# Performance work log

Hardware: AMD Instinct MI355X
Metric: run time of the kernel (lower is better)

The kernel has to match this reference:

```python
import jax, jax.numpy as jnp
import numpy as np

HEADS, DIM_HEAD, BLOCK, EPS = 16, 64, 16, 1e-8


def _hattn(x, w_qkv, w_out, b_out):
    b, n, dim = x.shape
    h, dh, bsz = HEADS, DIM_HEAD, BLOCK
    scale = dh ** -0.5
    # n is a power of two, so the module's pad-to-pow2 step is a no-op.
    qkv = x @ w_qkv  # [b, n, 3*h*dh]
    q, k, v = jnp.split(qkv, 3, axis=-1)

    def to_heads(t):  # [b, n, h*dh] -> [(b h), n, dh]
        return t.reshape(b, n, h, dh).transpose(0, 2, 1, 3).reshape(b * h, n, dh)

    q, k, v = to_heads(q) * scale, to_heads(k), to_heads(v)

    num_levels = int(np.log2(n // bsz)) - 1
    levels = [(q, k, v)]
    for _ in range(num_levels):  # coarsen: mean-pool q,k; sum-pool v (mask=None path)
        q = q.reshape(b * h, -1, 2, dh).mean(axis=2)
        k = k.reshape(b * h, -1, 2, dh).mean(axis=2)
        v = v.reshape(b * h, -1, 2, dh).sum(axis=2)
        levels.append((q, k, v))

    def flip_blocks(t):  # swap adjacent blocks along the block axis: [B, nb, z, d]
        B, nb, z, d = t.shape
        return t.reshape(B, nb // 2, 2, z, d)[:, :, ::-1].reshape(B, nb, z, d)

    Ys = []
    last = len(levels) - 1
    for ind, (ql, kl, vl) in enumerate(reversed(levels)):  # coarsest -> finest
        B, N, d = ql.shape
        qb = ql.reshape(B, N // bsz, bsz, d)
        kb = vb = None
        kb = kl.reshape(B, N // bsz, bsz, d)
        vb = vl.reshape(B, N // bsz, bsz, d)
        if ind != last:  # off-diagonal pairing at coarse levels
            kb, vb = flip_blocks(kb), flip_blocks(vb)
        S = jnp.einsum('bnid,bnjd->bnij', qb, kb)
        S = S - S.max(axis=-1, keepdims=True)
        A = jnp.exp(S)
        y = jnp.einsum('bnij,bnjd->bnid', A, vb)
        Ys.append((y.reshape(B, N, d), A.sum(-1).reshape(B, N)))

    Y, Asum = Ys[0]
    for y_l, a_l in Ys[1:]:  # upsample-and-accumulate across levels
        Y = jnp.repeat(Y, 2, axis=1) + y_l
        Asum = jnp.repeat(Asum, 2, axis=1) + a_l

    out = Y / (Asum + EPS)[..., None]  # [(b h), n, dh]
    out = out.reshape(b, h, n, dh).transpose(0, 2, 1, 3).reshape(b, n, h * dh)
    return out @ w_out + b_out


def setup_inputs() -> dict:
    key = jax.random.key(0)
    k1, k2, k3 = jax.random.split(key, 3)
    b, n, dim = 4, 8192, 1024
    inner = HEADS * DIM_HEAD
    x = jax.random.normal(k1, (b, n, dim), dtype=jnp.float32)
    w_qkv = jax.random.normal(k2, (dim, inner * 3), dtype=jnp.float32) * 0.02
    w_out = jax.random.normal(k3, (inner, dim), dtype=jnp.float32) * 0.02
    b_out = jnp.zeros((dim,), dtype=jnp.float32)
    return {"x": x, "w_qkv": w_qkv, "w_out": w_out, "b_out": b_out}


def reference(x, w_qkv, w_out, b_out):
    return _hattn(x, w_qkv, w_out, b_out)
```

## Files before the change

### kernel.cpp

```cpp
#include <hip/hip_runtime.h>

typedef unsigned short u16;
typedef unsigned int u32;
typedef __bf16 bf16x8 __attribute__((ext_vector_type(8)));
typedef float f32x4 __attribute__((ext_vector_type(4)));

__device__ inline float bf2f(u16 u) { u32 x = ((u32)u) << 16; return __uint_as_float(x); }
__device__ inline u16 f2bf(float f) {
  u32 x = __float_as_uint(f);
  u32 r = (x + 0x7FFFu + ((x >> 16) & 1u)) >> 16;
  return (u16)r;
}
__device__ inline u32 pack2(float lo, float hi) {
  return (u32)f2bf(lo) | ((u32)f2bf(hi) << 16);
}

__global__ __launch_bounds__(256) void cast_bf16(const float* __restrict__ s,
                                                 u16* __restrict__ d, int n4) {
  const float4* s4 = (const float4*)s;
  u32* d2 = (u32*)d;
  int i = blockIdx.x * 256 + threadIdx.x;
  int stride = gridDim.x * 256;
  for (; i < n4; i += stride) {
    float4 f = s4[i];
    d2[2 * i]     = pack2(f.x, f.y);
    d2[2 * i + 1] = pack2(f.z, f.w);
  }
}

__global__ __launch_bounds__(256) void transpose_cast(const float* __restrict__ src,
                                                      u16* __restrict__ dst, int R, int C) {
  __shared__ float tile[32][33];
  int bx = blockIdx.x, by = blockIdx.y;
  int tx = threadIdx.x & 31, ty = threadIdx.x >> 5;
  for (int rr = ty; rr < 32; rr += 8)
    tile[rr][tx] = src[(size_t)(by * 32 + rr) * C + bx * 32 + tx];
  __syncthreads();
  for (int rr = ty; rr < 32; rr += 8)
    dst[(size_t)(bx * 32 + rr) * R + by * 32 + tx] = f2bf(tile[tx][rr]);
}

#define MFMAQ(AF, BF, MO, NO)                                                     \
  _Pragma("unroll") for (int mf = 0; mf < 4; ++mf)                                \
  _Pragma("unroll") for (int nf = 0; nf < 2; ++nf)                                \
  _Pragma("unroll") for (int kq = 0; kq < 2; ++kq)                                \
    acc[(MO) + mf][(NO) + nf] = __builtin_amdgcn_mfma_f32_16x16x32_bf16(          \
        AF[mf][kq], BF[nf][kq], acc[(MO) + mf][(NO) + nf], 0, 0, 0);

#define PH_OPEN12                                                                 \
  asm volatile("s_waitcnt lgkmcnt(8)" ::: "memory");                              \
  __builtin_amdgcn_s_barrier();                                                   \
  asm volatile("s_waitcnt lgkmcnt(0)" ::: "memory");                              \
  __builtin_amdgcn_sched_barrier(0);                                              \
  __builtin_amdgcn_s_setprio(1);

#define PH_OPEN                                                                   \
  __builtin_amdgcn_s_barrier();                                                   \
  asm volatile("s_waitcnt lgkmcnt(0)" ::: "memory");                              \
  __builtin_amdgcn_sched_barrier(0);                                              \
  __builtin_amdgcn_s_setprio(1);

#define PH_CLOSE                                                                  \
  __builtin_amdgcn_s_setprio(0);                                                  \
  __builtin_amdgcn_s_barrier();                                                   \
  __builtin_amdgcn_sched_barrier(0);

#define PH_CLOSE_VM                                                               \
  __builtin_amdgcn_s_setprio(0);                                                  \
  asm volatile("s_waitcnt vmcnt(4)" ::: "memory");                                \
  __builtin_amdgcn_s_barrier();                                                   \
  __builtin_amdgcn_sched_barrier(0);

template <int EPI>
__global__ __launch_bounds__(512, 2) void gemm8p(
    const u16* __restrict__ A, const u16* __restrict__ Bt, int M, int N, int K, int NB,
    u16* __restrict__ q0, u16* __restrict__ k0, u16* __restrict__ v0,
    u16* __restrict__ q4, u16* __restrict__ k4, u16* __restrict__ v4,
    float* __restrict__ out, const float* __restrict__ bias) {
  __shared__ u16 lds[2][2][16384];
  const int tid = threadIdx.x;
  const int lane = tid & 63;
  const int wave = tid >> 6;
  const int wm = wave >> 2, wn = wave & 3;
  const int lr = lane & 15, lg = lane >> 4;

  const int nwg = gridDim.x;
  const int bid = blockIdx.x;
  const int swz = (bid & 7) * (nwg >> 3) + (bid >> 3);
  const int m0 = (swz / NB) * 256;
  const int n0 = (swz % NB) * 256;
  const int NT = K >> 6;
  const int NI = NT >> 1;

  auto stage_half = [&](int buf, int ht, int kt_) {
    const u16* src = (ht < 2) ? A : Bt;
    const int r0 = (ht < 2) ? m0 : n0;
    u16* ldsop = &lds[buf][ht >> 1][0];
#pragma unroll
    for (int ii = 0; ii < 2; ++ii) {
      int c2 = ((ht & 1) * 2 + ii) * 512 + tid;
      int row = c2 >> 3, ps = c2 & 7;
      int ks = ps ^ (row & 7);
      const u16* g = src + (size_t)(r0 + row) * K + kt_ + ks * 8;
      char* l = (char*)ldsop + (size_t)((((ht & 1) * 2 + ii) * 512 + (tid & ~63)) * 16);
      __builtin_amdgcn_global_load_lds((const __attribute__((address_space(1))) void*)g,
                                       (__attribute__((address_space(3))) void*)l, 16, 0, 0);
    }
  };
  auto rdA = [&](int c, int mf, int kq) -> bf16x8 {
    int rl = wm * 128 + mf * 16 + lr;
    int sl = (kq * 4 + lg) ^ (rl & 7);
    return *(const bf16x8*)(&lds[c][0][rl * 64 + sl * 8]);
  };
  auto rdB = [&](int c, int nf, int kq) -> bf16x8 {
    int rl = wn * 64 + nf * 16 + lr;
    int sl = (kq * 4 + lg) ^ (rl & 7);
    return *(const bf16x8*)(&lds[c][1][rl * 64 + sl * 8]);
  };

  f32x4 acc[8][4];
#pragma unroll
  for (int mf = 0; mf < 8; ++mf)
#pragma unroll
    for (int nf = 0; nf < 4; ++nf) acc[mf][nf] = f32x4{0.f, 0.f, 0.f, 0.f};

  stage_half(0, 2, 0); stage_half(0, 3, 0); stage_half(0, 0, 0); stage_half(0, 1, 0);
  stage_half(1, 2, 64); stage_half(1, 3, 64);
  asm volatile("s_waitcnt vmcnt(4)" ::: "memory");
  __builtin_amdgcn_s_barrier();
  __builtin_amdgcn_sched_barrier(0);

  bf16x8 afA[4][2], afB[4][2], bA[2][2], bB[2][2];
  for (int it = 0; it < NI; ++it) {
    const int kO  = (2 * it + 1) << 6;
    const int t2  = 2 * it + 2, t3 = 2 * it + 3;
    const int kE2 = ((t2 < NT) ? t2 : NT - 1) << 6;
    const int kO2 = ((t3 < NT) ? t3 : NT - 1) << 6;

#pragma unroll
    for (int mf = 0; mf < 4; ++mf) { afA[mf][0] = rdA(0, mf, 0); afA[mf][1] = rdA(0, mf, 1); }
#pragma unroll
    for (int nf = 0; nf < 2; ++nf) { bA[nf][0] = rdB(0, nf, 0); bA[nf][1] = rdB(0, nf, 1); }
    stage_half(1, 0, kO);
    PH_OPEN12 MFMAQ(afA, bA, 0, 0) PH_CLOSE
#pragma unroll
    for (int nf = 0; nf < 2; ++nf) { bB[nf][0] = rdB(0, 2 + nf, 0); bB[nf][1] = rdB(0, 2 + nf, 1); }
    stage_half(1, 1, kO);
    PH_OPEN MFMAQ(afA, bB, 0, 2) PH_CLOSE
#pragma unroll
    for (int mf = 0; mf < 4; ++mf) { afB[mf][0] = rdA(0, 4 + mf, 0); afB[mf][1] = rdA(0, 4 + mf, 1); }
    stage_half(0, 2, kE2);
    PH_OPEN MFMAQ(afB, bB, 4, 2) PH_CLOSE
    stage_half(0, 3, kE2);
    PH_OPEN MFMAQ(afB, bA, 4, 0) PH_CLOSE_VM
#pragma unroll
    for (int mf = 0; mf < 4; ++mf) { afA[mf][0] = rdA(1, mf, 0); afA[mf][1] = rdA(1, mf, 1); }
#pragma unroll
    for (int nf = 0; nf < 2; ++nf) { bA[nf][0] = rdB(1, nf, 0); bA[nf][1] = rdB(1, nf, 1); }
    stage_half(0, 0, kE2);
    PH_OPEN12 MFMAQ(afA, bA, 0, 0) PH_CLOSE
#pragma unroll
    for (int nf = 0; nf < 2; ++nf) { bB[nf][0] = rdB(1, 2 + nf, 0); bB[nf][1] = rdB(1, 2 + nf, 1); }
    stage_half(0, 1, kE2);
    PH_OPEN MFMAQ(afA, bB, 0, 2) PH_CLOSE
#pragma unroll
    for (int mf = 0; mf < 4; ++mf) { afB[mf][0] = rdA(1, 4 + mf, 0); afB[mf][1] = rdA(1, 4 + mf, 1); }
    stage_half(1, 2, kO2);
    PH_OPEN MFMAQ(afB, bB, 4, 2) PH_CLOSE
    stage_half(1, 3, kO2);
    PH_OPEN MFMAQ(afB, bA, 4, 0) PH_CLOSE_VM
  }
  asm volatile("s_waitcnt vmcnt(0)" ::: "memory");

#pragma unroll
  for (int mf = 0; mf < 8; ++mf) {
#pragma unroll
    for (int nf = 0; nf < 4; ++nf) {
      int col = n0 + wn * 64 + nf * 16 + lr;
      if (EPI == 0) {
        int p = col >> 10, cc = col & 1023;
        int h = cc >> 6, d = cc & 63;
        u16* dst = (p == 0) ? q0 : (p == 1) ? k0 : v0;
        float sc = (p == 0) ? 0.125f : 1.0f;
#pragma unroll
        for (int jj = 0; jj < 4; ++jj) {
          int row = m0 + wm * 128 + mf * 16 + lg * 4 + jj;
          int b = row >> 13, nn = row & 8191;
          dst[((size_t)((b << 4) + h) * 8192 + nn) * 64 + d] = f2bf(acc[mf][nf][jj] * sc);
        }
        float s4 = acc[mf][nf][0] + acc[mf][nf][1] + acc[mf][nf][2] + acc[mf][nf][3];
        s4 += __shfl_xor(s4, 16);
        s4 += __shfl_xor(s4, 32);
        if (lane < 16) {
          int row = m0 + wm * 128 + mf * 16;
          int b = row >> 13, n4 = (row & 8191) >> 4;
          u16* dst4 = (p == 0) ? q4 : (p == 1) ? k4 : v4;
          float val = (p == 2) ? s4 : s4 * 0.0625f;
          if (p == 0) val *= 0.125f;
          dst4[((size_t)((b << 4) + h) * 512 + n4) * 64 + d] = f2bf(val);
        }
      } else {
        float bv = bias[col];
#pragma unroll
        for (int jj = 0; jj < 4; ++jj) {
          int row = m0 + wm * 128 + mf * 16 + lg * 4 + jj;
          out[(size_t)row * N + col] = acc[mf][nf][jj] + bv;
        }
      }
    }
  }
}

__global__ __launch_bounds__(256) void pool_all4(
    const u16* __restrict__ q4, const u16* __restrict__ k4, const u16* __restrict__ v4,
    u16* __restrict__ qd, u16* __restrict__ kd, u16* __restrict__ vd) {
  int t = blockIdx.x * 256 + threadIdx.x;
  if (t >= 983040) return;
  int arr = blockIdx.y;
  int col = t & 31;
  int rr = t >> 5;
  int Bi = rr / 480;
  int r = rr % 480;
  int base, w, Nl;
  if (r < 256)      { base = 0;   w = 2;  Nl = 256; }
  else if (r < 384) { base = 256; w = 4;  Nl = 128; r -= 256; }
  else if (r < 448) { base = 384; w = 8;  Nl = 64;  r -= 384; }
  else              { base = 448; w = 16; Nl = 32;  r -= 448; }
  const u32* s = (const u32*)(arr == 0 ? q4 : arr == 1 ? k4 : v4);
  const u32* src = s + ((size_t)Bi * 512 + (size_t)r * w) * 32 + col;
  float lo = 0, hi = 0;
  for (int m = 0; m < w; ++m) {
    u32 u = src[(size_t)m * 32];
    lo += bf2f((u16)u); hi += bf2f((u16)(u >> 16));
  }
  float sc = (arr == 2) ? 1.0f : (1.0f / (float)w);
  u32* d = (u32*)(arr == 0 ? qd : arr == 1 ? kd : vd);
  d[(size_t)2048 * base + ((size_t)Bi * Nl + r) * 32 + col] = pack2(lo * sc, hi * sc);
}

__global__ __launch_bounds__(256) void hattn_coarse(
    const u16* __restrict__ q4, const u16* __restrict__ k4, const u16* __restrict__ v4,
    const u16* __restrict__ qc, const u16* __restrict__ kc, const u16* __restrict__ vc,
    float* __restrict__ ylvl, float* __restrict__ alvl) {
  __shared__ float qs[16][68], ks[16][68], vs[16][68];
  __shared__ float As[16][17];
  const int bx = blockIdx.x, Bi = blockIdx.y;
  int lvl, jb;
  if (bx < 32)      { lvl = 0; jb = bx; }
  else if (bx < 48) { lvl = 1; jb = bx - 32; }
  else if (bx < 56) { lvl = 2; jb = bx - 48; }
  else if (bx < 60) { lvl = 3; jb = bx - 56; }
  else              { lvl = 4; jb = bx - 60; }
  const int N = 512 >> lvl;
  const int srcb[5] = {0, 0, 256, 384, 448};
  const int offr[5] = {0, 512, 768, 896, 960};
  const u16* qp = (lvl == 0) ? q4 : qc + (size_t)4096 * srcb[lvl];
  const u16* kp = (lvl == 0) ? k4 : kc + (size_t)4096 * srcb[lvl];
  const u16* vp = (lvl == 0) ? v4 : vc + (size_t)4096 * srcb[lvl];
  const int tid = threadIdx.x;
  const int jk = jb ^ 1;
  const u32* qg = (const u32*)(qp + ((size_t)Bi * N + jb * 16) * 64);
  const u32* kg = (const u32*)(kp + ((size_t)Bi * N + jk * 16) * 64);
  const u32* vg = (const u32*)(vp + ((size_t)Bi * N + jk * 16) * 64);
#pragma unroll
  for (int u = tid; u < 512; u += 256) {
    int row = u >> 5, dp = (u & 31) * 2;
    u32 a = qg[u]; qs[row][dp] = bf2f((u16)a); qs[row][dp + 1] = bf2f((u16)(a >> 16));
    u32 b = kg[u]; ks[row][dp] = bf2f((u16)b); ks[row][dp + 1] = bf2f((u16)(b >> 16));
    u32 c = vg[u]; vs[row][dp] = bf2f((u16)c); vs[row][dp + 1] = bf2f((u16)(c >> 16));
  }
  __syncthreads();
  const int i = tid >> 4, j = tid & 15;
  float s = 0.f;
  const float4* qv = (const float4*)&qs[i][0];
  const float4* kv = (const float4*)&ks[j][0];
#pragma unroll
  for (int d4 = 0; d4 < 16; ++d4) {
    float4 a = qv[d4], b = kv[d4];
    s += a.x * b.x + a.y * b.y + a.z * b.z + a.w * b.w;
  }
  float mx = s;
#pragma unroll
  for (int off = 8; off; off >>= 1) mx = fmaxf(mx, __shfl_xor(mx, off, 16));
  float aexp = __expf(s - mx);
  float asum = aexp;
#pragma unroll
  for (int off = 8; off; off >>= 1) asum += __shfl_xor(asum, off, 16);
  As[i][j] = aexp;
  __syncthreads();
  float y0 = 0, y1 = 0, y2 = 0, y3 = 0;
  const int d0 = j * 4;
#pragma unroll
  for (int jj = 0; jj < 16; ++jj) {
    float av = As[i][jj];
    const float4 vv = *(const float4*)&vs[jj][d0];
    y0 += av * vv.x; y1 += av * vv.y; y2 += av * vv.z; y3 += av * vv.w;
  }
  const int nf = jb * 16 + i;
  float* yo = ylvl + (size_t)4096 * offr[lvl] + ((size_t)Bi * N + nf) * 64 + d0;
  yo[0] = y0; yo[1] = y1; yo[2] = y2; yo[3] = y3;
  if (j == 0) alvl[(size_t)64 * offr[lvl] + (size_t)Bi * N + nf] = asum;
}

union F8 { u32 w[4]; bf16x8 v; };

__device__ inline void acc_row8(const u16* p, float* a) {
  const u32* qw = (const u32*)p;
#pragma unroll
  for (int m = 0; m < 4; ++m) {
    u32 u = qw[m];
    a[2 * m]     += bf2f((u16)u);
    a[2 * m + 1] += bf2f((u16)(u >> 16));
  }
}
__device__ inline bf16x8 mk8(const float* a, float s) {
  F8 f;
#pragma unroll
  for (int m = 0; m < 4; ++m) f.w[m] = pack2(a[2 * m] * s, a[2 * m + 1] * s);
  return f.v;
}
__device__ inline bf16x8 pool_frag(const u16* arr, int row0, int cnt, int slotq, float scale) {
  float a[8] = {0, 0, 0, 0, 0, 0, 0, 0};
  for (int m = 0; m < cnt; ++m) {
    int r = row0 + m;
    acc_row8(arr + r * 64 + ((slotq ^ (r & 7)) * 8), a);
  }
  return mk8(a, scale);
}
__device__ inline bf16x8 rd_frag(const u16* arr, int r, int slotq) {
  return *(const bf16x8*)(arr + r * 64 + ((slotq ^ (r & 7)) * 8));
}
template <int LVL>
__device__ inline bf16x8 vt_frag(const u16* Vt, int c, int rbase) {
  float a[8] = {0, 0, 0, 0, 0, 0, 0, 0};
  const u32* p = (const u32*)(Vt + c * 266 + rbase);
#pragma unroll
  for (int g = 0; g < (1 << LVL); ++g) {
#pragma unroll
    for (int m = 0; m < 4; ++m) {
      u32 u = p[g * 4 + m];
      int t = g * 8 + 2 * m;
      a[t >> LVL]       += bf2f((u16)u);
      a[(t + 1) >> LVL] += bf2f((u16)(u >> 16));
    }
  }
  return mk8(a, 1.0f);
}

__device__ inline bf16x8 qk_softmax(bf16x8 ka0, bf16x8 ka1, bf16x8 qb0, bf16x8 qb1,
                                    int lane, float* asum_out) {
  f32x4 s = {0.f, 0.f, 0.f, 0.f};
  s = __builtin_amdgcn_mfma_f32_16x16x32_bf16(ka0, qb0, s, 0, 0, 0);
  s = __builtin_amdgcn_mfma_f32_16x16x32_bf16(ka1, qb1, s, 0, 0, 0);
  float mx = fmaxf(fmaxf(s[0], s[1]), fmaxf(s[2], s[3]));
  mx = fmaxf(mx, __shfl_xor(mx, 32));
  mx = fmaxf(mx, __shfl_xor(mx, 16));
  float p0 = __expf(s[0] - mx), p1 = __expf(s[1] - mx);
  float p2 = __expf(s[2] - mx), p3 = __expf(s[3] - mx);
  float as = p0 + p1 + p2 + p3;
  as += __shfl_xor(as, 32);
  as += __shfl_xor(as, 16);
  *asum_out = as;
  u32 pk01 = pack2(p0, p1), pk23 = pack2(p2, p3);
  int jq = lane & 15, lg = lane >> 4;
  int a1 = ((((lg * 2) * 16) + jq) & 63) << 2;
  int a2 = ((((lg * 2 + 1) * 16) + jq) & 63) << 2;
  F8 f;
  f.w[0] = (u32)__builtin_amdgcn_ds_bpermute(a1, (int)pk01);
  f.w[1] = (u32)__builtin_amdgcn_ds_bpermute(a1, (int)pk23);
  f.w[2] = (u32)__builtin_amdgcn_ds_bpermute(a2, (int)pk01);
  f.w[3] = (u32)__builtin_amdgcn_ds_bpermute(a2, (int)pk23);
  if (lg >= 2) { f.w[0] = 0; f.w[1] = 0; f.w[2] = 0; f.w[3] = 0; }
  return f.v;
}

__global__ __launch_bounds__(512, 1) void attn_fine(
    const u16* __restrict__ q, const u16* __restrict__ k, const u16* __restrict__ v,
    const float* __restrict__ ylvl, const float* __restrict__ alvl,
    u16* __restrict__ outA) {
  __shared__ u16 Qs[16384];
  __shared__ u16 Ks[16384];
  __shared__ u16 Vt[17024];
  __shared__ float Yc1[128][68];
  __shared__ float Yc2[64][68];
  __shared__ float Yc3[32][68];
  __shared__ float SUMc[224];
  const int tid = threadIdx.x;
  const int lane = tid & 63;
  const int wv = tid >> 6;
  const int j = lane & 15, lg = lane >> 4;
  const int ci = blockIdx.x, Bi = blockIdx.y;
  const size_t gbase = ((size_t)Bi * 8192 + (size_t)ci * 256) * 64;

#pragma unroll
  for (int it = 0; it < 4; ++it) {
    int sidx = it * 512 + tid;
    int row = sidx >> 3, ps = sidx & 7;
    int ks_ = ps ^ (row & 7);
    const u16* gq = q + gbase + (size_t)row * 64 + ks_ * 8;
    const u16* gk = k + gbase + (size_t)row * 64 + ks_ * 8;
    char* lq = (char*)Qs + (size_t)(it * 512 + (tid & ~63)) * 16;
    char* lk = (char*)Ks + (size_t)(it * 512 + (tid & ~63)) * 16;
    __builtin_amdgcn_global_load_lds((const __attribute__((address_space(1))) void*)gq,
                                     (__attribute__((address_space(3))) void*)lq, 16, 0, 0);
    __builtin_amdgcn_global_load_lds((const __attribute__((address_space(1))) void*)gk,
                                     (__attribute__((address_space(3))) void*)lk, 16, 0, 0);
  }
  {
    const uint4* gv = (const uint4*)(v + gbase);
    u32* Vt32 = (u32*)Vt;
#pragma unroll
    for (int it = 0; it < 2; ++it) {
      int i = it * 512 + tid;
      int r2 = i >> 3, cg = i & 7, c0 = cg * 8;
      uint4 a = gv[(size_t)(2 * r2) * 8 + cg];
      uint4 b = gv[(size_t)(2 * r2 + 1) * 8 + cg];
      const u16* pa = (const u16*)&a;
      const u16* pb = (const u16*)&b;
#pragma unroll
      for (int m = 0; m < 8; ++m)
        Vt32[(c0 + m) * 133 + r2] = (u32)pa[m] | ((u32)pb[m] << 16);
    }
  }
  __syncthreads();

  {
    int kb = wv ^ 1;
    bf16x8 ka0 = pool_frag(Ks, kb * 32 + 2 * j, 2, lg, 0.5f);
    bf16x8 ka1 = pool_frag(Ks, kb * 32 + 2 * j, 2, 4 + lg, 0.5f);
    bf16x8 qb0 = pool_frag(Qs, wv * 32 + 2 * j, 2, lg, 0.5f);
    bf16x8 qb1 = pool_frag(Qs, wv * 32 + 2 * j, 2, 4 + lg, 0.5f);
    float as;
    bf16x8 pa = qk_softmax(ka0, ka1, qb0, qb1, lane, &as);
    if (lg == 0) SUMc[wv * 16 + j] = as;
    int rb = kb * 32 + (lg & 1) * 16;
    f32x4 acc[4];
#pragma unroll
    for (int ch = 0; ch < 4; ++ch) {
      bf16x8 vb = vt_frag<1>(Vt, ch * 16 + j, rb);
      acc[ch] = __builtin_amdgcn_mfma_f32_16x16x32_bf16(pa, vb, f32x4{0.f,0.f,0.f,0.f}, 0, 0, 0);
    }
#pragma unroll
    for (int ch = 0; ch < 4; ++ch)
#pragma unroll
      for (int jj = 0; jj < 4; ++jj)
        Yc1[wv * 16 + lg * 4 + jj][ch * 16 + j] = acc[ch][jj];
  }
  if (wv < 4) {
    int kb = wv ^ 1;
    bf16x8 ka0 = pool_frag(Ks, kb * 64 + 4 * j, 4, lg, 0.25f);
    bf16x8 ka1 = pool_frag(Ks, kb * 64 + 4 * j, 4, 4 + lg, 0.25f);
    bf16x8 qb0 = pool_frag(Qs, wv * 64 + 4 * j, 4, lg, 0.25f);
    bf16x8 qb1 = pool_frag(Qs, wv * 64 + 4 * j, 4, 4 + lg, 0.25f);
    float as;
    bf16x8 pa = qk_softmax(ka0, ka1, qb0, qb1, lane, &as);
    if (lg == 0) SUMc[128 + wv * 16 + j] = as;
    int rb = kb * 64 + (lg & 1) * 32;
    f32x4 acc[4];
#pragma unroll
    for (int ch = 0; ch < 4; ++ch) {
      bf16x8 vb = vt_frag<2>(Vt, ch * 16 + j, rb);
      acc[ch] = __builtin_amdgcn_mfma_f32_16x16x32_bf16(pa, vb, f32x4{0.f,0.f,0.f,0.f}, 0, 0, 0);
    }
#pragma unroll
    for (int ch = 0; ch < 4; ++ch)
#pragma unroll
      for (int jj = 0; jj < 4; ++jj)
        Yc2[wv * 16 + lg * 4 + jj][ch * 16 + j] = acc[ch][jj];
  }
  if (wv >= 6) {
    int w3 = wv - 6;
    int kb = w3 ^ 1;
    bf16x8 ka0 = pool_frag(Ks, kb * 128 + 8 * j, 8, lg, 0.125f);
    bf16x8 ka1 = pool_frag(Ks, kb * 128 + 8 * j, 8, 4 + lg, 0.125f);
    bf16x8 qb0 = pool_frag(Qs, w3 * 128 + 8 * j, 8, lg, 0.125f);
    bf16x8 qb1 = pool_frag(Qs, w3 * 128 + 8 * j, 8, 4 + lg, 0.125f);
    float as;
    bf16x8 pa = qk_softmax(ka0, ka1, qb0, qb1, lane, &as);
    if (lg == 0) SUMc[192 + w3 * 16 + j] = as;
    int rb = kb * 128 + (lg & 1) * 64;
    f32x4 acc[4];
#pragma unroll
    for (int ch = 0; ch < 4; ++ch) {
      bf16x8 vb = vt_frag<3>(Vt, ch * 16 + j, rb);
      acc[ch] = __builtin_amdgcn_mfma_f32_16x16x32_bf16(pa, vb, f32x4{0.f,0.f,0.f,0.f}, 0, 0, 0);
    }
#pragma unroll
    for (int ch = 0; ch < 4; ++ch)
#pragma unroll
      for (int jj = 0; jj < 4; ++jj)
        Yc3[w3 * 16 + lg * 4 + jj][ch * 16 + j] = acc[ch][jj];
  }
  __syncthreads();

  const int batch = Bi >> 4, h = Bi & 15;
  const int offr[5] = {0, 512, 768, 896, 960};
#pragma unroll
  for (int bb = 0; bb < 2; ++bb) {
    int b = wv * 2 + bb;
    bf16x8 ka0 = rd_frag(Ks, b * 16 + j, lg);
    bf16x8 ka1 = rd_frag(Ks, b * 16 + j, 4 + lg);
    bf16x8 qb0 = rd_frag(Qs, b * 16 + j, lg);
    bf16x8 qb1 = rd_frag(Qs, b * 16 + j, 4 + lg);
    float as;
    bf16x8 pa = qk_softmax(ka0, ka1, qb0, qb1, lane, &as);
    float av[4];
#pragma unroll
    for (int jj = 0; jj < 4; ++jj)
      av[jj] = __int_as_float(__builtin_amdgcn_ds_bpermute((lg * 4 + jj) << 2,
                                                           __float_as_int(as)));
    int rb = b * 16 + (lg & 1) * 8;
    f32x4 acc[4];
#pragma unroll
    for (int ch = 0; ch < 4; ++ch) {
      bf16x8 vb = *(const bf16x8*)(Vt + (ch * 16 + j) * 266 + rb);
      acc[ch] = __builtin_amdgcn_mfma_f32_16x16x32_bf16(pa, vb, f32x4{0.f,0.f,0.f,0.f}, 0, 0, 0);
    }
    const int i4 = ci * 16 + b;
    float a4 = 0;
    float y4v[4] = {0, 0, 0, 0};
#pragma unroll
    for (int l = 0; l < 5; ++l) {
      int Rl = 512 >> l;
      size_t idx = (size_t)Bi * Rl + (i4 >> l);
      a4 += alvl[(size_t)64 * offr[l] + idx];
      const float* yp = ylvl + (size_t)4096 * offr[l] + idx * 64;
#pragma unroll
      for (int ch = 0; ch < 4; ++ch) y4v[ch] += yp[ch * 16 + j];
    }
#pragma unroll
    for (int jj = 0; jj < 4; ++jj) {
      int r0 = b * 16 + lg * 4 + jj;
      float at = av[jj] + SUMc[r0 >> 1] + SUMc[128 + (r0 >> 2)] + SUMc[192 + (r0 >> 3)] + a4;
      float inv = 1.0f / (at + 1e-8f);
      size_t n = (size_t)ci * 256 + r0;
      u16* orow = outA + ((size_t)batch * 8192 + n) * 1024 + h * 64 + j;
#pragma unroll
      for (int ch = 0; ch < 4; ++ch) {
        float yt = acc[ch][jj] + Yc1[r0 >> 1][ch * 16 + j] + Yc2[r0 >> 2][ch * 16 + j] +
                   Yc3[r0 >> 3][ch * 16 + j] + y4v[ch];
        orow[ch * 16] = f2bf(yt * inv);
      }
    }
  }
}

extern "C" void kernel_launch(void* const* d_in, const int* in_sizes, int n_in,
                              void* d_out, int out_size, void* d_ws, size_t ws_size,
                              hipStream_t stream) {
  const float* x = (const float*)d_in[0];
  const float* w_qkv = (const float*)d_in[1];
  const float* w_out = (const float*)d_in[2];
  const float* b_out = (const float*)d_in[3];
  float* out = (float*)d_out;

  char* ws = (char*)d_ws;
  size_t off = 0;
  auto alloc = [&](size_t bytes) -> char* {
    char* p = ws + off;
    off += (bytes + 255) & ~(size_t)255;
    return p;
  };
  u16* xb = (u16*)alloc(33554432ull * 2);
  u16* wqkvT = (u16*)alloc(3072ull * 1024 * 2);
  u16* woutT = (u16*)alloc(1024ull * 1024 * 2);
  u16* q0 = (u16*)alloc(67108864ull);
  u16* k0 = (u16*)alloc(67108864ull);
  u16* v0 = (u16*)alloc(67108864ull);
  u16* q4 = (u16*)alloc(4194304ull);
  u16* k4 = (u16*)alloc(4194304ull);
  u16* v4 = (u16*)alloc(4194304ull);
  u16* qc = (u16*)alloc(3932160ull);
  u16* kc = (u16*)alloc(3932160ull);
  u16* vc = (u16*)alloc(3932160ull);
  float* ylvl = (float*)alloc(16252928ull);
  float* alvl = (float*)alloc(253952ull);
  (void)ws_size; (void)in_sizes; (void)n_in; (void)out_size;

  cast_bf16<<<2048, 256, 0, stream>>>(x, xb, 33554432 / 4);
  transpose_cast<<<dim3(3072 / 32, 1024 / 32), 256, 0, stream>>>(w_qkv, wqkvT, 1024, 3072);
  transpose_cast<<<dim3(1024 / 32, 1024 / 32), 256, 0, stream>>>(w_out, woutT, 1024, 1024);

  gemm8p<0><<<1536, 512, 0, stream>>>(xb, wqkvT, 32768, 3072, 1024, 12,
                                      q0, k0, v0, q4, k4, v4, nullptr, nullptr);

  pool_all4<<<dim3(3840, 3), 256, 0, stream>>>(q4, k4, v4, qc, kc, vc);
  hattn_coarse<<<dim3(62, 64), 256, 0, stream>>>(q4, k4, v4, qc, kc, vc, ylvl, alvl);
  attn_fine<<<dim3(32, 64), 512, 0, stream>>>(q0, k0, v0, ylvl, alvl, xb);

  gemm8p<1><<<512, 512, 0, stream>>>(xb, woutT, 32768, 1024, 1024, 4,
                                     nullptr, nullptr, nullptr,
                                     nullptr, nullptr, nullptr, out, b_out);
}
```

Before: 469.6 us.

## Switch GEMM to 32x32x16 MFMA with reorganized four-phase pipeline

Replaces the 16x16x32 bf16 MFMA tiling in both projection GEMMs with 32x32x16 MFMA instructions. Accumulators become 4x2 f32x16 tiles, the LDS fragment reads and epilogue index math are rewritten to match, and the 8-phase schedule is collapsed into 4 phases that each issue a full half-tile of loads. Larger MFMA tiles need fewer LDS fragment reads per flop, but the coarser phase structure changes how loads overlap with compute and drops the partial lgkmcnt wait.

```diff
diff --git a/kernel.cpp b/kernel.cpp
--- a/kernel.cpp
+++ b/kernel.cpp
@@ -4,6 +4,7 @@
 typedef unsigned int u32;
 typedef __bf16 bf16x8 __attribute__((ext_vector_type(8)));
 typedef float f32x4 __attribute__((ext_vector_type(4)));
+typedef float f32x16 __attribute__((ext_vector_type(16)));
 
 __device__ inline float bf2f(u16 u) { u32 x = ((u32)u) << 16; return __uint_as_float(x); }
 __device__ inline u16 f2bf(float f) {
@@ -40,19 +41,11 @@
     dst[(size_t)(bx * 32 + rr) * R + by * 32 + tx] = f2bf(tile[tx][rr]);
 }
 
-#define MFMAQ(AF, BF, MO, NO)                                                     \
+#define MFMA32(AF, BF, NO)                                                        \
+  _Pragma("unroll") for (int ks = 0; ks < 4; ++ks)                                \
   _Pragma("unroll") for (int mf = 0; mf < 4; ++mf)                                \
-  _Pragma("unroll") for (int nf = 0; nf < 2; ++nf)                                \
-  _Pragma("unroll") for (int kq = 0; kq < 2; ++kq)                                \
-    acc[(MO) + mf][(NO) + nf] = __builtin_amdgcn_mfma_f32_16x16x32_bf16(          \
-        AF[mf][kq], BF[nf][kq], acc[(MO) + mf][(NO) + nf], 0, 0, 0);
-
-#define PH_OPEN12                                                                 \
-  asm volatile("s_waitcnt lgkmcnt(8)" ::: "memory");                              \
-  __builtin_amdgcn_s_barrier();                                                   \
-  asm volatile("s_waitcnt lgkmcnt(0)" ::: "memory");                              \
-  __builtin_amdgcn_sched_barrier(0);                                              \
-  __builtin_amdgcn_s_setprio(1);
+    acc[mf][NO] = __builtin_amdgcn_mfma_f32_32x32x16_bf16(                        \
+        AF[mf][ks], BF[ks], acc[mf][NO], 0, 0, 0);
 
 #define PH_OPEN                                                                   \
   __builtin_amdgcn_s_barrier();                                                   \
@@ -72,7 +65,7 @@
   __builtin_amdgcn_sched_barrier(0);
 
 template <int EPI>
-__global__ __launch_bounds__(512, 2) void gemm8p(
+__global__ __launch_bounds__(512, 2) void gemm32(
     const u16* __restrict__ A, const u16* __restrict__ Bt, int M, int N, int K, int NB,
     u16* __restrict__ q0, u16* __restrict__ k0, u16* __restrict__ v0,
     u16* __restrict__ q4, u16* __restrict__ k4, u16* __restrict__ v4,
@@ -82,7 +75,8 @@
   const int lane = tid & 63;
   const int wave = tid >> 6;
   const int wm = wave >> 2, wn = wave & 3;
-  const int lr = lane & 15, lg = lane >> 4;
+  const int l31 = lane & 31, hk = lane >> 5;
+  (void)M;
 
   const int nwg = gridDim.x;
   const int bid = blockIdx.x;
@@ -107,30 +101,34 @@
                                        (__attribute__((address_space(3))) void*)l, 16, 0, 0);
     }
   };
-  auto rdA = [&](int c, int mf, int kq) -> bf16x8 {
-    int rl = wm * 128 + mf * 16 + lr;
-    int sl = (kq * 4 + lg) ^ (rl & 7);
+  auto rdA = [&](int c, int mf, int ks) -> bf16x8 {
+    int rl = wm * 128 + mf * 32 + l31;
+    int sl = (ks * 2 + hk) ^ (rl & 7);
     return *(const bf16x8*)(&lds[c][0][rl * 64 + sl * 8]);
   };
-  auto rdB = [&](int c, int nf, int kq) -> bf16x8 {
-    int rl = wn * 64 + nf * 16 + lr;
-    int sl = (kq * 4 + lg) ^ (rl & 7);
+  auto rdB = [&](int c, int nf, int ks) -> bf16x8 {
+    int rl = wn * 64 + nf * 32 + l31;
+    int sl = (ks * 2 + hk) ^ (rl & 7);
     return *(const bf16x8*)(&lds[c][1][rl * 64 + sl * 8]);
   };
 
-  f32x4 acc[8][4];
-#pragma unroll
-  for (int mf = 0; mf < 8; ++mf)
-#pragma unroll
-    for (int nf = 0; nf < 4; ++nf) acc[mf][nf] = f32x4{0.f, 0.f, 0.f, 0.f};
-
-  stage_half(0, 2, 0); stage_half(0, 3, 0); stage_half(0, 0, 0); stage_half(0, 1, 0);
-  stage_half(1, 2, 64); stage_half(1, 3, 64);
+  f32x16 acc[4][2];
+#pragma unroll
+  for (int mf = 0; mf < 4; ++mf)
+#pragma unroll
+    for (int nf = 0; nf < 2; ++nf)
+#pragma unroll
+      for (int r = 0; r < 16; ++r) acc[mf][nf][r] = 0.f;
+
+  const int k1t = ((NT > 1) ? 1 : 0) << 6;
+  stage_half(0, 0, 0); stage_half(0, 1, 0);
+  stage_half(0, 2, 0); stage_half(0, 3, 0);
+  stage_half(1, 0, k1t); stage_half(1, 1, k1t);
   asm volatile("s_waitcnt vmcnt(4)" ::: "memory");
   __builtin_amdgcn_s_barrier();
   __builtin_amdgcn_sched_barrier(0);
 
-  bf16x8 afA[4][2], afB[4][2], bA[2][2], bB[2][2];
+  bf16x8 af[4][4], bfr[4];
   for (int it = 0; it < NI; ++it) {
     const int kO  = (2 * it + 1) << 6;
     const int t2  = 2 * it + 2, t3 = 2 * it + 3;
@@ -138,73 +136,71 @@
     const int kO2 = ((t3 < NT) ? t3 : NT - 1) << 6;
 
 #pragma unroll
-    for (int mf = 0; mf < 4; ++mf) { afA[mf][0] = rdA(0, mf, 0); afA[mf][1] = rdA(0, mf, 1); }
-#pragma unroll
-    for (int nf = 0; nf < 2; ++nf) { bA[nf][0] = rdB(0, nf, 0); bA[nf][1] = rdB(0, nf, 1); }
-    stage_half(1, 0, kO);
-    PH_OPEN12 MFMAQ(afA, bA, 0, 0) PH_CLOSE
-#pragma unroll
-    for (int nf = 0; nf < 2; ++nf) { bB[nf][0] = rdB(0, 2 + nf, 0); bB[nf][1] = rdB(0, 2 + nf, 1); }
-    stage_half(1, 1, kO);
-    PH_OPEN MFMAQ(afA, bB, 0, 2) PH_CLOSE
-#pragma unroll
-    for (int mf = 0; mf < 4; ++mf) { afB[mf][0] = rdA(0, 4 + mf, 0); afB[mf][1] = rdA(0, 4 + mf, 1); }
-    stage_half(0, 2, kE2);
-    PH_OPEN MFMAQ(afB, bB, 4, 2) PH_CLOSE
-    stage_half(0, 3, kE2);
-    PH_OPEN MFMAQ(afB, bA, 4, 0) PH_CLOSE_VM
-#pragma unroll
-    for (int mf = 0; mf < 4; ++mf) { afA[mf][0] = rdA(1, mf, 0); afA[mf][1] = rdA(1, mf, 1); }
-#pragma unroll
-    for (int nf = 0; nf < 2; ++nf) { bA[nf][0] = rdB(1, nf, 0); bA[nf][1] = rdB(1, nf, 1); }
-    stage_half(0, 0, kE2);
-    PH_OPEN12 MFMAQ(afA, bA, 0, 0) PH_CLOSE
-#pragma unroll
-    for (int nf = 0; nf < 2; ++nf) { bB[nf][0] = rdB(1, 2 + nf, 0); bB[nf][1] = rdB(1, 2 + nf, 1); }
-    stage_half(0, 1, kE2);
-    PH_OPEN MFMAQ(afA, bB, 0, 2) PH_CLOSE
-#pragma unroll
-    for (int mf = 0; mf < 4; ++mf) { afB[mf][0] = rdA(1, 4 + mf, 0); afB[mf][1] = rdA(1, 4 + mf, 1); }
-    stage_half(1, 2, kO2);
-    PH_OPEN MFMAQ(afB, bB, 4, 2) PH_CLOSE
-    stage_half(1, 3, kO2);
-    PH_OPEN MFMAQ(afB, bA, 4, 0) PH_CLOSE_VM
+    for (int mf = 0; mf < 4; ++mf)
+#pragma unroll
+      for (int ks = 0; ks < 4; ++ks) af[mf][ks] = rdA(0, mf, ks);
+#pragma unroll
+    for (int ks = 0; ks < 4; ++ks) bfr[ks] = rdB(0, 0, ks);
+    stage_half(1, 2, kO); stage_half(1, 3, kO);
+    PH_OPEN MFMA32(af, bfr, 0) PH_CLOSE
+#pragma unroll
+    for (int ks = 0; ks < 4; ++ks) bfr[ks] = rdB(0, 1, ks);
+    stage_half(0, 0, kE2); stage_half(0, 1, kE2);
+    PH_OPEN MFMA32(af, bfr, 1) PH_CLOSE_VM
+#pragma unroll
+    for (int mf = 0; mf < 4; ++mf)
+#pragma unroll
+      for (int ks = 0; ks < 4; ++ks) af[mf][ks] = rdA(1, mf, ks);
+#pragma unroll
+    for (int ks = 0; ks < 4; ++ks) bfr[ks] = rdB(1, 0, ks);
+    stage_half(0, 2, kE2); stage_half(0, 3, kE2);
+    PH_OPEN MFMA32(af, bfr, 0) PH_CLOSE
+#pragma unroll
+    for (int ks = 0; ks < 4; ++ks) bfr[ks] = rdB(1, 1, ks);
+    stage_half(1, 0, kO2); stage_half(1, 1, kO2);
+    PH_OPEN MFMA32(af, bfr, 1) PH_CLOSE_VM
   }
   asm volatile("s_waitcnt vmcnt(0)" ::: "memory");
 
 #pragma unroll
-  for (int mf = 0; mf < 8; ++mf) {
-#pragma unroll
-    for (int nf = 0; nf < 4; ++nf) {
-      int col = n0 + wn * 64 + nf * 16 + lr;
+  for (int mf = 0; mf < 4; ++mf) {
+#pragma unroll
+    for (int nf = 0; nf < 2; ++nf) {
+      int col = n0 + wn * 64 + nf * 32 + l31;
       if (EPI == 0) {
         int p = col >> 10, cc = col & 1023;
         int h = cc >> 6, d = cc & 63;
         u16* dst = (p == 0) ? q0 : (p == 1) ? k0 : v0;
         float sc = (p == 0) ? 0.125f : 1.0f;
 #pragma unroll
-        for (int jj = 0; jj < 4; ++jj) {
-          int row = m0 + wm * 128 + mf * 16 + lg * 4 + jj;
+        for (int r = 0; r < 16; ++r) {
+          int row = m0 + wm * 128 + mf * 32 + (r & 3) + 8 * (r >> 2) + 4 * hk;
           int b = row >> 13, nn = row & 8191;
-          dst[((size_t)((b << 4) + h) * 8192 + nn) * 64 + d] = f2bf(acc[mf][nf][jj] * sc);
+          dst[((size_t)((b << 4) + h) * 8192 + nn) * 64 + d] = f2bf(acc[mf][nf][r] * sc);
         }
-        float s4 = acc[mf][nf][0] + acc[mf][nf][1] + acc[mf][nf][2] + acc[mf][nf][3];
-        s4 += __shfl_xor(s4, 16);
-        s4 += __shfl_xor(s4, 32);
-        if (lane < 16) {
-          int row = m0 + wm * 128 + mf * 16;
-          int b = row >> 13, n4 = (row & 8191) >> 4;
+        float sA = 0.f, sB = 0.f;
+#pragma unroll
+        for (int r = 0; r < 8; ++r) { sA += acc[mf][nf][r]; sB += acc[mf][nf][8 + r]; }
+        sA += __shfl_xor(sA, 32);
+        sB += __shfl_xor(sB, 32);
+        if (lane < 32) {
           u16* dst4 = (p == 0) ? q4 : (p == 1) ? k4 : v4;
-          float val = (p == 2) ? s4 : s4 * 0.0625f;
-          if (p == 0) val *= 0.125f;
-          dst4[((size_t)((b << 4) + h) * 512 + n4) * 64 + d] = f2bf(val);
+#pragma unroll
+          for (int hf = 0; hf < 2; ++hf) {
+            float sv = hf ? sB : sA;
+            int row = m0 + wm * 128 + mf * 32 + hf * 16;
+            int b = row >> 13, n4 = (row & 8191) >> 4;
+            float val = (p == 2) ? sv : sv * 0.0625f;
+            if (p == 0) val *= 0.125f;
+            dst4[((size_t)((b << 4) + h) * 512 + n4) * 64 + d] = f2bf(val);
+          }
         }
       } else {
         float bv = bias[col];
 #pragma unroll
-        for (int jj = 0; jj < 4; ++jj) {
-          int row = m0 + wm * 128 + mf * 16 + lg * 4 + jj;
-          out[(size_t)row * N + col] = acc[mf][nf][jj] + bv;
+        for (int r = 0; r < 16; ++r) {
+          int row = m0 + wm * 128 + mf * 32 + (r & 3) + 8 * (r >> 2) + 4 * hk;
+          out[(size_t)row * N + col] = acc[mf][nf][r] + bv;
         }
       }
     }
@@ -581,14 +577,14 @@
   transpose_cast<<<dim3(3072 / 32, 1024 / 32), 256, 0, stream>>>(w_qkv, wqkvT, 1024, 3072);
   transpose_cast<<<dim3(1024 / 32, 1024 / 32), 256, 0, stream>>>(w_out, woutT, 1024, 1024);
 
-  gemm8p<0><<<1536, 512, 0, stream>>>(xb, wqkvT, 32768, 3072, 1024, 12,
+  gemm32<0><<<1536, 512, 0, stream>>>(xb, wqkvT, 32768, 3072, 1024, 12,
                                       q0, k0, v0, q4, k4, v4, nullptr, nullptr);
 
   pool_all4<<<dim3(3840, 3), 256, 0, stream>>>(q4, k4, v4, qc, kc, vc);
   hattn_coarse<<<dim3(62, 64), 256, 0, stream>>>(q4, k4, v4, qc, kc, vc, ylvl, alvl);
   attn_fine<<<dim3(32, 64), 512, 0, stream>>>(q0, k0, v0, ylvl, alvl, xb);
 
-  gemm8p<1><<<512, 512, 0, stream>>>(xb, woutT, 32768, 1024, 1024, 4,
+  gemm32<1><<<512, 512, 0, stream>>>(xb, woutT, 32768, 1024, 1024, 4,
                                      nullptr, nullptr, nullptr,
                                      nullptr, nullptr, nullptr, out, b_out);
 }
```

Result: slower. 661.9 us (+41.0%).
